# Kernel tuning notes

Measured on AMD Instinct MI355X. Metric: run time of the kernel, lower is better.

Reference implementation:

```python
import jax, jax.numpy as jnp
import numpy as np

N_NODES = 50000
N_EDGES = 800000
N_GRAPHS = 64
NUM_CLASSES = 10


def _glorot(key, shape):
    fan_in, fan_out = shape
    lim = np.sqrt(6.0 / (fan_in + fan_out)).astype(np.float32)
    return jax.random.uniform(key, shape, jnp.float32, -lim, lim)


def setup_inputs() -> dict:
    key = jax.random.key(0)
    ks = jax.random.split(key, 12)
    x = jax.random.normal(ks[0], (N_NODES, 5), jnp.float32)
    edge_index = jax.random.randint(ks[1], (2, N_EDGES), 0, N_NODES, jnp.int64)
    batch = jnp.sort(jax.random.randint(ks[2], (N_NODES,), 0, N_GRAPHS, jnp.int64))
    dims = [5, 32, 64, 128, 256]
    params = {}
    for i in range(4):
        params[f"W{i+1}"] = _glorot(ks[3 + i], (dims[i], dims[i + 1]))
        params[f"b{i+1}"] = jnp.zeros((dims[i + 1],), jnp.float32)
    params["fcW"] = _glorot(ks[7], (256, NUM_CLASSES))
    params["fcb"] = jnp.zeros((NUM_CLASSES,), jnp.float32)
    return {"x": x, "edge_index": edge_index, "batch": batch, **params}


def reference(x, edge_index, batch, W1, b1, W2, b2, W3, b3, W4, b4, fcW, fcb):
    n = x.shape[0]
    loop = jnp.arange(n, dtype=edge_index.dtype)
    src = jnp.concatenate([edge_index[0], loop])  # source nodes (+ self loops)
    dst = jnp.concatenate([edge_index[1], loop])  # target nodes (+ self loops)
    # symmetric GCN normalization: D^{-1/2} (A+I) D^{-1/2}
    deg = jax.ops.segment_sum(jnp.ones_like(dst, x.dtype), dst, num_segments=n)
    dinv = jax.lax.rsqrt(deg)  # deg >= 1 due to self loops
    norm = (dinv[src] * dinv[dst])[:, None]

    def gcn(h, W, b):
        h = h @ W                                        # dense transform
        agg = jax.ops.segment_sum(h[src] * norm, dst, num_segments=n)
        return agg + b

    h = jax.nn.relu(gcn(x, W1, b1))
    h = jax.nn.relu(gcn(h, W2, b2))
    h = jax.nn.relu(gcn(h, W3, b3))
    h = jax.nn.relu(gcn(h, W4, b4))                      # [n, 256]

    # global mean pool over graphs
    counts = jax.ops.segment_sum(jnp.ones((n,), h.dtype), batch, num_segments=N_GRAPHS)
    pooled = jax.ops.segment_sum(h, batch, num_segments=N_GRAPHS)
    pooled = pooled / jnp.maximum(counts, 1.0)[:, None]  # [G, 256]

    return jax.nn.log_softmax(pooled @ fcW + fcb, axis=-1)
```

## Files before the change

### kernel.cpp

```cpp
#include <hip/hip_runtime.h>
#include <hip/hip_bf16.h>
#include <math.h>

#define N_NODES 50000
#define N_EDGES 800000
#define N_GRAPHS 64
#define NUM_CLASSES 10
#define BIN_W 256
#define NBINS ((N_NODES + BIN_W - 1) / BIN_W)
#define CHUNK 4096
#define NCHUNKS ((N_EDGES + CHUNK - 1) / CHUNK)
#define CAP 8192
#define CPB 64
#define PACK_BLOCKS 21

typedef __attribute__((ext_vector_type(8))) short bf16x8;
typedef __attribute__((ext_vector_type(4))) float f32x4;

__device__ inline unsigned short f2bf(float f) {
    unsigned int u = __float_as_uint(f);
    u += 0x7fffu + ((u >> 16) & 1u);
    return (unsigned short)(u >> 16);
}
__device__ inline float bf2f(unsigned short v) {
    return __uint_as_float((unsigned int)v << 16);
}
__device__ inline void bf8_unpack(uint4 v, float* o) {
    o[0] = __uint_as_float(v.x << 16); o[1] = __uint_as_float(v.x & 0xffff0000u);
    o[2] = __uint_as_float(v.y << 16); o[3] = __uint_as_float(v.y & 0xffff0000u);
    o[4] = __uint_as_float(v.z << 16); o[5] = __uint_as_float(v.z & 0xffff0000u);
    o[6] = __uint_as_float(v.w << 16); o[7] = __uint_as_float(v.w & 0xffff0000u);
}
__device__ inline unsigned int pack2(float a, float b) {
    return (unsigned int)f2bf(a) | ((unsigned int)f2bf(b) << 16);
}

template<int K, int N>
__device__ void packW_dev(const float* __restrict__ W, unsigned short* __restrict__ Wp,
                          int bid, int l) {
    constexpr int KT = K / 32;
    int kt = bid % KT, nt = bid / KT;
    int m = l & 15, quad = l >> 4;
    #pragma unroll
    for (int j = 0; j < 8; j++) {
        int k = kt * 32 + quad * 8 + j;
        int n = nt * 16 + m;
        Wp[((size_t)bid * 64 + l) * 8 + j] = f2bf(W[(size_t)k * N + n]);
    }
}

__global__ __launch_bounds__(256) void k_binscatter(const int* __restrict__ src,
                                                    const int* __restrict__ dst,
                                                    unsigned short* __restrict__ cnt,
                                                    unsigned int* __restrict__ binned,
                                                    const float* __restrict__ W2,
                                                    const float* __restrict__ W3,
                                                    const float* __restrict__ W4,
                                                    unsigned short* wp2, unsigned short* wp3,
                                                    unsigned short* wp4) {
    int bid = blockIdx.x, t = threadIdx.x;
    if (bid >= NCHUNKS) {
        int w = (bid - NCHUNKS) * 4 + (t >> 6);
        int lane = t & 63;
        if (w < 4)       packW_dev<32, 64>(W2, wp2, w, lane);
        else if (w < 20) packW_dev<64, 128>(W3, wp3, w - 4, lane);
        else if (w < 84) packW_dev<128, 256>(W4, wp4, w - 20, lane);
        return;
    }
    __shared__ int hist[NBINS];
    __shared__ int off[NBINS];
    __shared__ int bump[NBINS];
    __shared__ unsigned int stage[CHUNK];
    __shared__ unsigned char sbin[CHUNK];
    int base = bid * CHUNK;
    int total = N_EDGES - base; if (total > CHUNK) total = CHUNK;
    for (int i = t; i < NBINS; i += 256) { hist[i] = 0; bump[i] = 0; }
    __syncthreads();
    int es[16], ed[16];
    #pragma unroll
    for (int i = 0; i < 16; i++) {
        int e = base + t + i * 256;
        if (e < N_EDGES) { es[i] = src[e]; ed[i] = dst[e]; }
        else ed[i] = -1;
    }
    #pragma unroll
    for (int i = 0; i < 16; i++)
        if (ed[i] >= 0) atomicAdd(&hist[ed[i] >> 8], 1);
    __syncthreads();
    {
        __shared__ int s[256];
        int v = (t < NBINS) ? hist[t] : 0;
        s[t] = v; __syncthreads();
        for (int o = 1; o < 256; o <<= 1) {
            int x = (t >= o) ? s[t - o] : 0;
            __syncthreads();
            s[t] += x;
            __syncthreads();
        }
        if (t < NBINS) off[t] = s[t] - v;
    }
    __syncthreads();
    #pragma unroll
    for (int i = 0; i < 16; i++) {
        if (ed[i] >= 0) {
            int b = ed[i] >> 8;
            int lpos = off[b] + atomicAdd(&bump[b], 1);
            stage[lpos] = ((unsigned int)(ed[i] & 255) << 16) | (unsigned int)es[i];
            sbin[lpos] = (unsigned char)b;
        }
    }
    __syncthreads();
    for (int j = t; j < total; j += 256) {
        int b = sbin[j];
        int pos = j - off[b];
        if (pos < CPB)
            binned[((size_t)b * NCHUNKS + bid) * CPB + pos] = stage[j];
    }
    if (t < NBINS) {
        int h = hist[t]; if (h > CPB) h = CPB;
        cnt[(size_t)bid * NBINS + t] = (unsigned short)h;
    }
}

__global__ __launch_bounds__(256) void k_csr(const unsigned int* __restrict__ binned,
                                             const unsigned short* __restrict__ cnt,
                                             unsigned int* __restrict__ row_ptr,
                                             float* __restrict__ dinv,
                                             unsigned short* __restrict__ csr16,
                                             const float* __restrict__ x,
                                             float* __restrict__ x5) {
    __shared__ unsigned int stage[CAP];
    __shared__ int coff[256];
    __shared__ int deg[BIN_W];
    __shared__ int off[BIN_W];
    __shared__ int bump[BIN_W];
    __shared__ int s_total;
    int b = blockIdx.x;
    int t = threadIdx.x;
    deg[t] = 0; bump[t] = 0;
    int myc = (t < NCHUNKS) ? (int)cnt[(size_t)t * NBINS + b] : 0;
    {
        __shared__ int s[256];
        s[t] = myc; __syncthreads();
        for (int o = 1; o < 256; o <<= 1) {
            int v = (t >= o) ? s[t - o] : 0;
            __syncthreads();
            s[t] += v;
            __syncthreads();
        }
        coff[t] = s[t] - myc;
        if (t == 255) s_total = s[255];
    }
    __syncthreads();
    int total = s_total; if (total > CAP) total = CAP;
    if (t < NCHUNKS && myc > 0) {
        const unsigned int* seg = &binned[((size_t)b * NCHUNKS + t) * CPB];
        int o0 = coff[t];
        for (int j = 0; j < myc && o0 + j < CAP; j++)
            stage[o0 + j] = seg[j];
    }
    __syncthreads();
    for (int e = t; e < total; e += 256)
        atomicAdd(&deg[stage[e] >> 16], 1);
    __syncthreads();
    {
        __shared__ int s[256];
        int v = deg[t];
        s[t] = v; __syncthreads();
        for (int o = 1; o < 256; o <<= 1) {
            int x2 = (t >= o) ? s[t - o] : 0;
            __syncthreads();
            s[t] += x2;
            __syncthreads();
        }
        off[t] = s[t] - v;
    }
    __syncthreads();
    int e0 = b * CAP;
    int node = b * BIN_W + t;
    if (node < N_NODES) {
        float di = rsqrtf((float)(deg[t] + 1));
        row_ptr[node] = (unsigned int)(e0 + off[t]) | ((unsigned int)deg[t] << 21);
        dinv[node] = di;
        #pragma unroll
        for (int f = 0; f < 5; f++)
            x5[node * 5 + f] = di * x[node * 5 + f];
    }
    for (int e = t; e < total; e += 256) {
        unsigned int v = stage[e];
        int dl = v >> 16;
        int pos = e0 + off[dl] + atomicAdd(&bump[dl], 1);
        csr16[pos] = (unsigned short)(v & 0xffffu);
    }
}

__global__ __launch_bounds__(256) void k_layer1(const float* __restrict__ x5,
                                                const unsigned int* __restrict__ row_ptr,
                                                const unsigned short* __restrict__ csr16,
                                                const float* __restrict__ dinv,
                                                const float* __restrict__ W1,
                                                const float* __restrict__ b1,
                                                unsigned short* __restrict__ Hout) {
    __shared__ float A5[32 * 6];
    __shared__ float Ws[160];
    __shared__ float bs[32];
    int t = threadIdx.x;
    int row0 = blockIdx.x * 32;
    if (t < 160) Ws[t] = W1[t];
    if (t >= 224) bs[t - 224] = b1[t - 224];
    int nl = t >> 3, f = t & 7;
    int node = row0 + nl;
    float val = 0.0f;
    float dnode = 0.0f;
    if (node < N_NODES) dnode = dinv[node];
    if (f < 5 && node < N_NODES) {
        float acc0 = x5[node * 5 + f], acc1 = 0.0f;
        unsigned int v = row_ptr[node];
        int e0 = (int)(v & 0x1FFFFFu);
        int e1 = e0 + (int)(v >> 21);
        int e = e0;
        for (; e + 7 < e1; e += 8) {
            int s0 = csr16[e], s1 = csr16[e + 1], s2 = csr16[e + 2], s3 = csr16[e + 3];
            int s4 = csr16[e + 4], s5 = csr16[e + 5], s6 = csr16[e + 6], s7 = csr16[e + 7];
            float x0 = x5[s0 * 5 + f], x1 = x5[s1 * 5 + f];
            float x2 = x5[s2 * 5 + f], x3 = x5[s3 * 5 + f];
            float x4 = x5[s4 * 5 + f], x5v = x5[s5 * 5 + f];
            float x6 = x5[s6 * 5 + f], x7 = x5[s7 * 5 + f];
            acc0 += (x0 + x2) + (x4 + x6);
            acc1 += (x1 + x3) + (x5v + x7);
        }
        for (; e + 3 < e1; e += 4) {
            int s0 = csr16[e], s1 = csr16[e + 1], s2 = csr16[e + 2], s3 = csr16[e + 3];
            float x0 = x5[s0 * 5 + f], x1 = x5[s1 * 5 + f];
            float x2 = x5[s2 * 5 + f], x3 = x5[s3 * 5 + f];
            acc0 += x0 + x2;
            acc1 += x1 + x3;
        }
        for (; e < e1; e++) acc0 += x5[csr16[e] * 5 + f];
        val = dnode * (acc0 + acc1);
    }
    if (f < 5) A5[nl * 6 + f] = val;
    __syncthreads();
    int j0 = (t & 7) * 4;
    int node2 = row0 + (t >> 3);
    float d2 = (node2 < N_NODES) ? dinv[node2] : 0.0f;
    float a[5];
    #pragma unroll
    for (int k = 0; k < 5; k++) a[k] = A5[(t >> 3) * 6 + k];
    ushort4 o;
    unsigned short* op = (unsigned short*)&o;
    #pragma unroll
    for (int c = 0; c < 4; c++) {
        float acc = bs[j0 + c];
        #pragma unroll
        for (int k = 0; k < 5; k++) acc += a[k] * Ws[k * 32 + j0 + c];
        op[c] = f2bf(d2 * fmaxf(acc, 0.0f));
    }
    if (node2 < N_NODES) *(ushort4*)&Hout[(size_t)node2 * 32 + j0] = o;
}

template<int K, int N, bool SCALE, bool POOL>
__global__ __launch_bounds__(256) void k_fused(const unsigned short* __restrict__ Hin,
                                               const unsigned int* __restrict__ row_ptr,
                                               const unsigned short* __restrict__ csr16,
                                               const float* __restrict__ dinv,
                                               const unsigned short* __restrict__ Wp,
                                               const float* __restrict__ bias,
                                               unsigned short* __restrict__ C,
                                               const int* __restrict__ batch,
                                               float* __restrict__ pooled) {
    constexpr int KT = K / 32, NT = N / 16, DV = K / 8;
    constexpr int NPB = 2048 / K;
    constexpr int TM = NPB / 16;
    constexpr int KP = K + 8;
    __shared__ unsigned short As[NPB * KP];
    __shared__ int bb[POOL ? NPB : 4];
    int t = threadIdx.x;
    int row0 = blockIdx.x * NPB;
    if constexpr (POOL) {
        if (t < NPB) bb[t] = batch[min(row0 + t, N_NODES - 1)];
    }
    {
        int nl = t / DV, f = t % DV;
        int node = row0 + nl;
        const uint4* h4 = (const uint4*)Hin;
        uint4 o = {0u, 0u, 0u, 0u};
        if (node < N_NODES) {
            float di = dinv[node];
            float acc0[8], acc1[8];
            bf8_unpack(h4[(size_t)node * DV + f], acc0);
            #pragma unroll
            for (int i = 0; i < 8; i++) acc1[i] = 0.0f;
            unsigned int rv = row_ptr[node];
            int e0 = (int)(rv & 0x1FFFFFu);
            int e1 = e0 + (int)(rv >> 21);
            int e = e0;
            for (; e + 3 < e1; e += 4) {
                int s0 = csr16[e], s1 = csr16[e + 1], s2 = csr16[e + 2], s3 = csr16[e + 3];
                uint4 u0 = h4[(size_t)s0 * DV + f];
                uint4 u1 = h4[(size_t)s1 * DV + f];
                uint4 u2 = h4[(size_t)s2 * DV + f];
                uint4 u3 = h4[(size_t)s3 * DV + f];
                float t0[8], t1[8], t2[8], t3[8];
                bf8_unpack(u0, t0); bf8_unpack(u1, t1);
                bf8_unpack(u2, t2); bf8_unpack(u3, t3);
                #pragma unroll
                for (int i = 0; i < 8; i++) {
                    acc0[i] += t0[i] + t2[i];
                    acc1[i] += t1[i] + t3[i];
                }
            }
            for (; e + 1 < e1; e += 2) {
                int s0 = csr16[e], s1 = csr16[e + 1];
                uint4 u0 = h4[(size_t)s0 * DV + f];
                uint4 u1 = h4[(size_t)s1 * DV + f];
                float t0[8], t1[8];
                bf8_unpack(u0, t0);
                bf8_unpack(u1, t1);
                #pragma unroll
                for (int i = 0; i < 8; i++) { acc0[i] += t0[i]; acc1[i] += t1[i]; }
            }
            if (e < e1) {
                float t0[8];
                bf8_unpack(h4[(size_t)csr16[e] * DV + f], t0);
                #pragma unroll
                for (int i = 0; i < 8; i++) acc0[i] += t0[i];
            }
            o.x = pack2(di * (acc0[0] + acc1[0]), di * (acc0[1] + acc1[1]));
            o.y = pack2(di * (acc0[2] + acc1[2]), di * (acc0[3] + acc1[3]));
            o.z = pack2(di * (acc0[4] + acc1[4]), di * (acc0[5] + acc1[5]));
            o.w = pack2(di * (acc0[6] + acc1[6]), di * (acc0[7] + acc1[7]));
        }
        *(uint4*)&As[nl * KP + f * 8] = o;
    }
    __syncthreads();
    int wave = t >> 6, lane = t & 63;
    int m = lane & 15, quad = lane >> 4;
    bf16x8 a[TM][KT];
    float dr[TM][4];
    #pragma unroll
    for (int mt = 0; mt < TM; mt++) {
        #pragma unroll
        for (int kt = 0; kt < KT; kt++)
            a[mt][kt] = *(const bf16x8*)&As[(mt * 16 + m) * KP + kt * 32 + quad * 8];
        #pragma unroll
        for (int r = 0; r < 4; r++) {
            int row = row0 + mt * 16 + quad * 4 + r;
            dr[mt][r] = (SCALE && row < N_NODES) ? dinv[row] : 1.0f;
        }
    }
    const bf16x8* Bp = (const bf16x8*)Wp;
    int g0 = 0, g1 = 0;
    if constexpr (POOL) { g0 = bb[0]; g1 = bb[NPB - 1]; }
    for (int j = wave; j < TM * NT; j += 4) {
        int mt = j % TM, nt = j / TM;
        f32x4 c = {0.f, 0.f, 0.f, 0.f};
        #pragma unroll
        for (int kt = 0; kt < KT; kt++)
            c = __builtin_amdgcn_mfma_f32_16x16x32_bf16(a[mt][kt],
                    Bp[(size_t)(nt * KT + kt) * 64 + lane], c, 0, 0, 0);
        int col = nt * 16 + m;
        float bv = bias[col];
        if constexpr (POOL) {
            float acc0 = 0.0f, acc1 = 0.0f;
            #pragma unroll
            for (int r = 0; r < 4; r++) {
                int rl = mt * 16 + quad * 4 + r;
                int row = row0 + rl;
                if (row < N_NODES) {
                    float v = fmaxf(c[r] + bv, 0.0f);
                    int g = bb[rl];
                    if (g == g0) acc0 += v;
                    else if (g == g1) acc1 += v;
                    else atomicAdd(&pooled[(size_t)g * 256 + col], v);
                }
            }
            acc0 += __shfl_xor(acc0, 32); acc0 += __shfl_xor(acc0, 16);
            acc1 += __shfl_xor(acc1, 32); acc1 += __shfl_xor(acc1, 16);
            if (lane < 16) {
                atomicAdd(&pooled[(size_t)g0 * 256 + col], acc0);
                if (g1 != g0) atomicAdd(&pooled[(size_t)g1 * 256 + col], acc1);
            }
        } else {
            #pragma unroll
            for (int r = 0; r < 4; r++) {
                int row = row0 + mt * 16 + quad * 4 + r;
                if (row < N_NODES) {
                    float v = fmaxf(c[r] + bv, 0.0f);
                    if constexpr (SCALE) v *= dr[mt][r];
                    C[(size_t)row * N + col] = f2bf(v);
                }
            }
        }
    }
}

__global__ void k_final(const float* __restrict__ pooled, const int* __restrict__ batch,
                        const float* __restrict__ fcW, const float* __restrict__ fcb,
                        float* __restrict__ out) {
    int g = blockIdx.x;
    int t = threadIdx.x;
    float cnt = 0.0f;
    if (t == 0) {
        int lo = 0, hi = N_NODES;
        while (lo < hi) { int m = (lo + hi) >> 1; if (batch[m] < g) lo = m + 1; else hi = m; }
        int start = lo;
        lo = 0; hi = N_NODES;
        while (lo < hi) { int m = (lo + hi) >> 1; if (batch[m] < g + 1) lo = m + 1; else hi = m; }
        cnt = (float)(lo - start);
    }
    float inv = 1.0f / fmaxf(__shfl(cnt, 0), 1.0f);
    float p[4];
    #pragma unroll
    for (int m = 0; m < 4; m++) p[m] = pooled[g * 256 + t + 64 * m];
    float logits[NUM_CLASSES];
    #pragma unroll
    for (int j = 0; j < NUM_CLASSES; j++) {
        float s = 0.0f;
        #pragma unroll
        for (int m = 0; m < 4; m++) s += p[m] * fcW[(t + 64 * m) * NUM_CLASSES + j];
        for (int off = 32; off > 0; off >>= 1) s += __shfl_xor(s, off);
        logits[j] = s * inv + fcb[j];
    }
    float mx = logits[0];
    #pragma unroll
    for (int j = 1; j < NUM_CLASSES; j++) mx = fmaxf(mx, logits[j]);
    float se = 0.0f;
    #pragma unroll
    for (int j = 0; j < NUM_CLASSES; j++) se += expf(logits[j] - mx);
    float lse = mx + logf(se);
    if (t < NUM_CLASSES) out[g * NUM_CLASSES + t] = logits[t] - lse;
}

extern "C" void kernel_launch(void* const* d_in, const int* in_sizes, int n_in,
                              void* d_out, int out_size, void* d_ws, size_t ws_size,
                              hipStream_t stream) {
    const float* x     = (const float*)d_in[0];
    const int*   ei    = (const int*)d_in[1];
    const int*   src   = ei;
    const int*   dst   = ei + N_EDGES;
    const int*   batch = (const int*)d_in[2];
    const float* W1 = (const float*)d_in[3];  const float* b1 = (const float*)d_in[4];
    const float* W2 = (const float*)d_in[5];  const float* b2 = (const float*)d_in[6];
    const float* W3 = (const float*)d_in[7];  const float* b3 = (const float*)d_in[8];
    const float* W4 = (const float*)d_in[9];  const float* b4 = (const float*)d_in[10];
    const float* fcW = (const float*)d_in[11]; const float* fcb = (const float*)d_in[12];
    float* out = (float*)d_out;

    char* ws = (char*)d_ws;
    unsigned short* buf1 = (unsigned short*)ws; ws += (size_t)N_NODES * 256 * 2;
    unsigned short* buf2 = (unsigned short*)ws; ws += (size_t)N_NODES * 256 * 2;
    float* dinv     = (float*)ws; ws += (size_t)N_NODES * 4;
    float* x5       = (float*)ws; ws += (size_t)N_NODES * 5 * 4 + 16;
    unsigned int* row_ptr = (unsigned int*)ws; ws += (size_t)(N_NODES + 4) * 4;
    unsigned short* csr16 = (unsigned short*)ws; ws += (size_t)NBINS * CAP * 2;
    unsigned int* binned = (unsigned int*)ws; ws += (size_t)NBINS * NCHUNKS * CPB * 4;
    unsigned short* cnt = (unsigned short*)ws; ws += (size_t)NCHUNKS * NBINS * 2 + 16;
    float* pooled   = (float*)ws; ws += (size_t)N_GRAPHS * 256 * 4;
    unsigned short* wp2 = (unsigned short*)ws; ws += 32 * 64 * 2;
    unsigned short* wp3 = (unsigned short*)ws; ws += 64 * 128 * 2;
    unsigned short* wp4 = (unsigned short*)ws; ws += 128 * 256 * 2;

    const int TB = 256;
    k_binscatter<<<NCHUNKS + PACK_BLOCKS, TB, 0, stream>>>(src, dst, cnt, binned,
                                                           W2, W3, W4, wp2, wp3, wp4);
    k_csr<<<NBINS, TB, 0, stream>>>(binned, cnt, row_ptr, dinv, csr16, x, x5);

    k_layer1<<<(N_NODES + 31) / 32, TB, 0, stream>>>(x5, row_ptr, csr16, dinv, W1, b1, buf1);
    k_fused<32, 64, true, false><<<(N_NODES + 63) / 64, TB, 0, stream>>>(
        buf1, row_ptr, csr16, dinv, wp2, b2, buf2, nullptr, nullptr);
    k_fused<64, 128, true, false><<<(N_NODES + 31) / 32, TB, 0, stream>>>(
        buf2, row_ptr, csr16, dinv, wp3, b3, buf1, nullptr, nullptr);
    k_fused<128, 256, false, true><<<(N_NODES + 15) / 16, TB, 0, stream>>>(
        buf1, row_ptr, csr16, dinv, wp4, b4, nullptr, batch, pooled);

    k_final<<<N_GRAPHS, 64, 0, stream>>>(pooled, batch, fcW, fcb, out);
}
```

Measured before the change: 194.1 us.

## Sort nodes by degree within each bin to balance gather work per block

```diff
diff --git a/kernel.cpp b/kernel.cpp
--- a/kernel.cpp
+++ b/kernel.cpp
@@ -8,6 +8,7 @@
 #define NUM_CLASSES 10
 #define BIN_W 256
 #define NBINS ((N_NODES + BIN_W - 1) / BIN_W)
+#define NPERM (NBINS * BIN_W)
 #define CHUNK 4096
 #define NCHUNKS ((N_EDGES + CHUNK - 1) / CHUNK)
 #define CAP 8192
@@ -128,7 +129,8 @@
                                              float* __restrict__ dinv,
                                              unsigned short* __restrict__ csr16,
                                              const float* __restrict__ x,
-                                             float* __restrict__ x5) {
+                                             float* __restrict__ x5,
+                                             int* __restrict__ perm) {
     __shared__ unsigned int stage[CAP];
     __shared__ int coff[256];
     __shared__ int deg[BIN_W];
@@ -192,6 +194,26 @@
         int pos = e0 + off[dl] + atomicAdd(&bump[dl], 1);
         csr16[pos] = (unsigned short)(v & 0xffffu);
     }
+    __syncthreads();
+    __shared__ int dh[64];
+    __shared__ int dof[64];
+    if (t < 64) dh[t] = 0;
+    __syncthreads();
+    int bkt = deg[t] > 63 ? 63 : deg[t];
+    atomicAdd(&dh[bkt], 1);
+    __syncthreads();
+    if (t < 64) {
+        int v = dh[t];
+        #pragma unroll
+        for (int o = 1; o < 64; o <<= 1) {
+            int u = __shfl_up(v, o);
+            if (t >= o) v += u;
+        }
+        dof[t] = v - dh[t];
+    }
+    __syncthreads();
+    int pos = atomicAdd(&dof[bkt], 1);
+    perm[b * BIN_W + pos] = node;
 }
 
 __global__ __launch_bounds__(256) void k_layer1(const float* __restrict__ x5,
@@ -200,16 +222,20 @@
                                                 const float* __restrict__ dinv,
                                                 const float* __restrict__ W1,
                                                 const float* __restrict__ b1,
-                                                unsigned short* __restrict__ Hout) {
+                                                unsigned short* __restrict__ Hout,
+                                                const int* __restrict__ perm) {
     __shared__ float A5[32 * 6];
     __shared__ float Ws[160];
     __shared__ float bs[32];
+    __shared__ int prn[32];
     int t = threadIdx.x;
     int row0 = blockIdx.x * 32;
     if (t < 160) Ws[t] = W1[t];
     if (t >= 224) bs[t - 224] = b1[t - 224];
+    if (t < 32) prn[t] = perm[row0 + t];
+    __syncthreads();
     int nl = t >> 3, f = t & 7;
-    int node = row0 + nl;
+    int node = prn[nl];
     float val = 0.0f;
     float dnode = 0.0f;
     if (node < N_NODES) dnode = dinv[node];
@@ -242,7 +268,7 @@
     if (f < 5) A5[nl * 6 + f] = val;
     __syncthreads();
     int j0 = (t & 7) * 4;
-    int node2 = row0 + (t >> 3);
+    int node2 = prn[t >> 3];
     float d2 = (node2 < N_NODES) ? dinv[node2] : 0.0f;
     float a[5];
     #pragma unroll
@@ -268,21 +294,25 @@
                                                const float* __restrict__ bias,
                                                unsigned short* __restrict__ C,
                                                const int* __restrict__ batch,
-                                               float* __restrict__ pooled) {
+                                               float* __restrict__ pooled,
+                                               const int* __restrict__ perm) {
     constexpr int KT = K / 32, NT = N / 16, DV = K / 8;
     constexpr int NPB = 2048 / K;
     constexpr int TM = NPB / 16;
     constexpr int KP = K + 8;
     __shared__ unsigned short As[NPB * KP];
     __shared__ int bb[POOL ? NPB : 4];
+    __shared__ int pr[NPB];
     int t = threadIdx.x;
     int row0 = blockIdx.x * NPB;
+    if (t < NPB) pr[t] = perm[row0 + t];
+    __syncthreads();
     if constexpr (POOL) {
-        if (t < NPB) bb[t] = batch[min(row0 + t, N_NODES - 1)];
+        if (t < NPB) bb[t] = batch[min(pr[t], N_NODES - 1)];
     }
     {
         int nl = t / DV, f = t % DV;
-        int node = row0 + nl;
+        int node = pr[nl];
         const uint4* h4 = (const uint4*)Hin;
         uint4 o = {0u, 0u, 0u, 0u};
         if (node < N_NODES) {
@@ -345,13 +375,17 @@
             a[mt][kt] = *(const bf16x8*)&As[(mt * 16 + m) * KP + kt * 32 + quad * 8];
         #pragma unroll
         for (int r = 0; r < 4; r++) {
-            int row = row0 + mt * 16 + quad * 4 + r;
-            dr[mt][r] = (SCALE && row < N_NODES) ? dinv[row] : 1.0f;
+            int p = pr[mt * 16 + quad * 4 + r];
+            dr[mt][r] = (SCALE && p < N_NODES) ? dinv[p] : 1.0f;
         }
     }
     const bf16x8* Bp = (const bf16x8*)Wp;
     int g0 = 0, g1 = 0;
-    if constexpr (POOL) { g0 = bb[0]; g1 = bb[NPB - 1]; }
+    if constexpr (POOL) {
+        int bb0 = row0 & ~(BIN_W - 1);
+        g0 = batch[bb0];
+        g1 = batch[min(bb0 + BIN_W - 1, N_NODES - 1)];
+    }
     for (int j = wave; j < TM * NT; j += 4) {
         int mt = j % TM, nt = j / TM;
         f32x4 c = {0.f, 0.f, 0.f, 0.f};
@@ -366,7 +400,7 @@
             #pragma unroll
             for (int r = 0; r < 4; r++) {
                 int rl = mt * 16 + quad * 4 + r;
-                int row = row0 + rl;
+                int row = pr[rl];
                 if (row < N_NODES) {
                     float v = fmaxf(c[r] + bv, 0.0f);
                     int g = bb[rl];
@@ -384,7 +418,7 @@
         } else {
             #pragma unroll
             for (int r = 0; r < 4; r++) {
-                int row = row0 + mt * 16 + quad * 4 + r;
+                int row = pr[mt * 16 + quad * 4 + r];
                 if (row < N_NODES) {
                     float v = fmaxf(c[r] + bv, 0.0f);
                     if constexpr (SCALE) v *= dr[mt][r];
@@ -460,19 +494,20 @@
     unsigned short* wp2 = (unsigned short*)ws; ws += 32 * 64 * 2;
     unsigned short* wp3 = (unsigned short*)ws; ws += 64 * 128 * 2;
     unsigned short* wp4 = (unsigned short*)ws; ws += 128 * 256 * 2;
+    int* perm = (int*)ws; ws += (size_t)NPERM * 4;
 
     const int TB = 256;
     k_binscatter<<<NCHUNKS + PACK_BLOCKS, TB, 0, stream>>>(src, dst, cnt, binned,
                                                            W2, W3, W4, wp2, wp3, wp4);
-    k_csr<<<NBINS, TB, 0, stream>>>(binned, cnt, row_ptr, dinv, csr16, x, x5);
-
-    k_layer1<<<(N_NODES + 31) / 32, TB, 0, stream>>>(x5, row_ptr, csr16, dinv, W1, b1, buf1);
-    k_fused<32, 64, true, false><<<(N_NODES + 63) / 64, TB, 0, stream>>>(
-        buf1, row_ptr, csr16, dinv, wp2, b2, buf2, nullptr, nullptr);
-    k_fused<64, 128, true, false><<<(N_NODES + 31) / 32, TB, 0, stream>>>(
-        buf2, row_ptr, csr16, dinv, wp3, b3, buf1, nullptr, nullptr);
-    k_fused<128, 256, false, true><<<(N_NODES + 15) / 16, TB, 0, stream>>>(
-        buf1, row_ptr, csr16, dinv, wp4, b4, nullptr, batch, pooled);
+    k_csr<<<NBINS, TB, 0, stream>>>(binned, cnt, row_ptr, dinv, csr16, x, x5, perm);
+
+    k_layer1<<<NPERM / 32, TB, 0, stream>>>(x5, row_ptr, csr16, dinv, W1, b1, buf1, perm);
+    k_fused<32, 64, true, false><<<NPERM / 64, TB, 0, stream>>>(
+        buf1, row_ptr, csr16, dinv, wp2, b2, buf2, nullptr, nullptr, perm);
+    k_fused<64, 128, true, false><<<NPERM / 32, TB, 0, stream>>>(
+        buf2, row_ptr, csr16, dinv, wp3, b3, buf1, nullptr, nullptr, perm);
+    k_fused<128, 256, false, true><<<NPERM / 16, TB, 0, stream>>>(
+        buf1, row_ptr, csr16, dinv, wp4, b4, nullptr, batch, pooled, perm);
 
     k_final<<<N_GRAPHS, 64, 0, stream>>>(pooled, batch, fcW, fcb, out);
 }
```

After: 206.6 us. 1.06x slower.
